# Kernel tuning notes

Hardware: AMD Instinct MI355X
Metric: run time of the kernel (lower is better)

Reference implementation:

```python
import jax, jax.numpy as jnp
from jax import lax
import numpy as np

K = 3  # kernel size for both convs


def setup_inputs() -> dict:
    key = jax.random.key(0)
    k1, k2, k3, k4, k5 = jax.random.split(key, 5)
    x = jax.random.normal(k1, (8, 3, 384, 384), dtype=jnp.float32)
    # offset-producing conv: 18 = 2*3*3 offset channels for a 3x3 deform kernel
    w1 = jax.random.normal(k2, (18, 3, K, K), dtype=jnp.float32) * 0.05
    b1 = jax.random.normal(k3, (18,), dtype=jnp.float32) * 0.05
    # deformable conv weight/bias: in=3, out=3, 3x3
    w2 = jax.random.normal(k4, (3, 3, K, K), dtype=jnp.float32) * 0.2
    b2 = jax.random.normal(k5, (3,), dtype=jnp.float32) * 0.05
    return {"x": x, "w1": w1, "b1": b1, "w2": w2, "b2": b2}


def _deform_conv2d(x, offset, w, b):
    # x: [B,C,H,W], offset: [B, 2*K*K, Ho, Wo] (per-tap (dy,dx) interleaved),
    # w: [Co,C,K,K], b: [Co]. stride=1, pad=0, dilation=1, zero-padding bilinear.
    B, C, H, W = x.shape
    KK = K * K
    Ho, Wo = H - (K - 1), W - (K - 1)
    off = offset.reshape(B, KK, 2, Ho, Wo)
    dy, dx = off[:, :, 0], off[:, :, 1]                      # [B,KK,Ho,Wo]

    kh = jnp.repeat(jnp.arange(K, dtype=jnp.float32), K)     # [KK] kernel row
    kw = jnp.tile(jnp.arange(K, dtype=jnp.float32), K)       # [KK] kernel col
    base_y = jnp.arange(Ho, dtype=jnp.float32)[None, :, None] + kh[:, None, None]  # [KK,Ho,1]
    base_x = jnp.arange(Wo, dtype=jnp.float32)[None, None, :] + kw[:, None, None]  # [KK,1,Wo]
    py = base_y[None] + dy                                   # [B,KK,Ho,Wo]
    px = base_x[None] + dx

    y0 = jnp.floor(py)
    x0 = jnp.floor(px)
    wy = py - y0
    wx = px - x0

    x_flat = x.reshape(B, C, H * W)
    N = KK * Ho * Wo

    def gather_corner(yc, xc, wgt):
        valid = (yc >= 0) & (yc <= H - 1) & (xc >= 0) & (xc <= W - 1)
        yi = jnp.clip(yc, 0, H - 1).astype(jnp.int32)
        xi = jnp.clip(xc, 0, W - 1).astype(jnp.int32)
        idx = (yi * W + xi).reshape(B, 1, N)
        g = jnp.take_along_axis(x_flat, idx, axis=2)          # [B,C,N]
        return g * (wgt * valid.astype(x.dtype)).reshape(B, 1, N)

    val = gather_corner(y0, x0, (1 - wy) * (1 - wx))
    val = val + gather_corner(y0, x0 + 1, (1 - wy) * wx)
    val = val + gather_corner(y0 + 1, x0, wy * (1 - wx))
    val = val + gather_corner(y0 + 1, x0 + 1, wy * wx)
    val = val.reshape(B, C, KK, Ho, Wo)

    out = jnp.einsum('bckhw,ock->bohw', val, w.reshape(w.shape[0], C, KK))
    return out + b[None, :, None, None]


def reference(x, w1, b1, w2, b2):
    offset = lax.conv_general_dilated(
        x, w1, window_strides=(1, 1), padding='VALID',
        dimension_numbers=('NCHW', 'OIHW', 'NCHW')) + b1[None, :, None, None]
    return _deform_conv2d(x, offset, w2, b2)
```

## Files before the change

### kernel.cpp

```cpp
#include <hip/hip_runtime.h>


#define BB 8
#define HH 384
#define WW 384
#define HO 382
#define WO 382
#define HW (HH * WW)
#define PIX_PER_BATCH (HO * WO)
#define BLOCKS_PER_BATCH ((PIX_PER_BATCH + 255) / 256)
#define TR_BLOCKS_PER_BATCH (HW / 256)

typedef float v2f __attribute__((ext_vector_type(2), aligned(4)));
typedef float v4f __attribute__((ext_vector_type(4), aligned(16)));

static __device__ __forceinline__ v2f fma2(v2f a, v2f b, v2f c) {
    return __builtin_elementwise_fma(a, b, c);
}
static __device__ __forceinline__ v4f fma4(v4f a, v4f b, v4f c) {
    return __builtin_elementwise_fma(a, b, c);
}

__global__ __launch_bounds__(256) void nchw_to_nhwc4(
    const float* __restrict__ x, v4f* __restrict__ xt)
{
    const int b    = blockIdx.x & 7;
    const int tile = blockIdx.x >> 3;
    const int idx  = tile * 256 + threadIdx.x;
    const float* xb = x + (long)b * 3 * HW;
    v4f v;
    v.x = xb[idx];
    v.y = xb[HW + idx];
    v.z = xb[2 * HW + idx];
    v.w = 0.f;
    xt[(long)b * HW + idx] = v;
}

__global__ __launch_bounds__(256, 5) void deform_fused_nhwc(
    const v4f* __restrict__ xt,
    const float* __restrict__ w1,
    const float* __restrict__ b1,
    const float* __restrict__ w2,
    const float* __restrict__ b2,
    float* __restrict__ out)
{
    __shared__ float s_w1p[486];
    __shared__ float s_b1[18];
    __shared__ float s_w2p[54];
    __shared__ float s_w2s[27];
    __shared__ float s_b2[3];

    for (int i = threadIdx.x; i < 486; i += 256) {
        const int oc = i / 27, rem = i % 27, c = rem / 9, j = rem % 9;
        const int k = oc >> 1, comp = oc & 1;
        s_w1p[((j * 3 + c) * 9 + k) * 2 + comp] = w1[i];
    }
    if (threadIdx.x < 81) {
        const int i = threadIdx.x;
        const int o = i / 27, c = (i % 27) / 9, k = i % 9;
        if (o < 2) s_w2p[(k * 3 + c) * 2 + o] = w2[i];
        else       s_w2s[k * 3 + c] = w2[i];
    }
    if (threadIdx.x < 18) s_b1[threadIdx.x] = b1[threadIdx.x];
    if (threadIdx.x < 3)  s_b2[threadIdx.x] = b2[threadIdx.x];
    __syncthreads();

    const int b    = blockIdx.x & 7;
    const int tile = blockIdx.x >> 3;
    const int idx  = tile * 256 + threadIdx.x;
    if (idx >= PIX_PER_BATCH) return;

    const int wo = idx % WO;
    const int ho = idx / WO;

    const v4f* xtb = xt + (long)b * HW;

    v2f off2[9];
#pragma unroll
    for (int k = 0; k < 9; ++k) {
        v2f v; v.x = s_b1[2 * k]; v.y = s_b1[2 * k + 1];
        off2[k] = v;
    }

    const v2f* w1p = (const v2f*)s_w1p;
#pragma unroll
    for (int j = 0; j < 9; ++j) {
        const int i = j / 3, jj = j % 3;
        const v4f q = xtb[(ho + i) * WW + (wo + jj)];
#pragma unroll
        for (int c = 0; c < 3; ++c) {
            const float xc = (c == 0) ? q.x : (c == 1) ? q.y : q.z;
            v2f xcv; xcv.x = xc; xcv.y = xc;
            const v2f* wrow = w1p + (j * 3 + c) * 9;
#pragma unroll
            for (int k = 0; k < 9; ++k)
                off2[k] = fma2(xcv, wrow[k], off2[k]);
        }
    }

    float acc0 = s_b2[0], acc1 = s_b2[1], acc2 = s_b2[2];
    const v2f* w2p = (const v2f*)s_w2p;

#pragma unroll
    for (int k = 0; k < 9; ++k) {
        const int kh = k / 3, kw = k % 3;
        v2f pos; pos.x = (float)(ho + kh); pos.y = (float)(wo + kw);
        pos += off2[k];
        const v2f fl = __builtin_elementwise_floor(pos);
        const v2f fr = pos - fl;
        const int y0 = (int)fl.x;
        const int x0 = (int)fl.y;

        const int ry0 = min(max(y0, 0), HH - 1);
        const int ry1 = min(max(y0 + 1, 0), HH - 1);
        const int xbs = min(max(x0, 0), WW - 2);

        const bool vy0 = (y0 >= 0) & (y0 <= HH - 1);
        const bool vy1 = (y0 >= -1) & (y0 <= HH - 2);
        const bool vx0 = (x0 >= 0) & (x0 <= WW - 1);
        const bool vx1 = (x0 >= -1) & (x0 <= WW - 2);
        const float wy0m = vy0 ? (1.f - fr.x) : 0.f;
        const float wy1m = vy1 ? fr.x : 0.f;
        const float wx0m = vx0 ? (1.f - fr.y) : 0.f;
        const float wx1m = vx1 ? fr.y : 0.f;

        const bool selA = (x0 >= WW - 1);
        const bool selB = (x0 >= 0);
        const float e0 = (selA ? 0.f : wx0m) + (selB ? 0.f : wx1m);
        const float e1 = (selA ? wx0m : 0.f) + (selB ? wx1m : 0.f);
        const float g00 = wy0m * e0, g01 = wy0m * e1;
        const float g10 = wy1m * e0, g11 = wy1m * e1;

        const int o0 = ry0 * WW + xbs;
        const int o1 = ry1 * WW + xbs;

        const v4f q00 = xtb[o0];
        const v4f q01 = xtb[o0 + 1];
        const v4f q10 = xtb[o1];
        const v4f q11 = xtb[o1 + 1];

        v4f gv; gv.x = g00; gv.y = g00; gv.z = g00; gv.w = g00;
        v4f t4 = gv * q00;
        gv.x = g01; gv.y = g01; gv.z = g01; gv.w = g01;
        t4 = fma4(gv, q01, t4);
        gv.x = g10; gv.y = g10; gv.z = g10; gv.w = g10;
        t4 = fma4(gv, q10, t4);
        gv.x = g11; gv.y = g11; gv.z = g11; gv.w = g11;
        t4 = fma4(gv, q11, t4);

        const float v0 = t4.x, v1 = t4.y, v2v = t4.z;

        v2f acc01; acc01.x = acc0; acc01.y = acc1;
        v2f vv;
        vv.x = v0;  vv.y = v0;  acc01 = fma2(vv, w2p[k * 3 + 0], acc01);
        vv.x = v1;  vv.y = v1;  acc01 = fma2(vv, w2p[k * 3 + 1], acc01);
        vv.x = v2v; vv.y = v2v; acc01 = fma2(vv, w2p[k * 3 + 2], acc01);
        acc0 = acc01.x; acc1 = acc01.y;
        acc2 = fmaf(s_w2s[k * 3 + 0], v0, acc2);
        acc2 = fmaf(s_w2s[k * 3 + 1], v1, acc2);
        acc2 = fmaf(s_w2s[k * 3 + 2], v2v, acc2);
    }

    const long obase = ((long)(b * 3) * HO + ho) * WO + wo;
    __builtin_nontemporal_store(acc0, out + obase);
    __builtin_nontemporal_store(acc1, out + obase + (long)HO * WO);
    __builtin_nontemporal_store(acc2, out + obase + 2L * HO * WO);
}

__global__ __launch_bounds__(256, 6) void deform_fused_fallback(
    const float* __restrict__ x,
    const float* __restrict__ w1,
    const float* __restrict__ b1,
    const float* __restrict__ w2,
    const float* __restrict__ b2,
    float* __restrict__ out)
{
    __shared__ float s_w1p[486];
    __shared__ float s_b1[18];
    __shared__ float s_w2p[54];
    __shared__ float s_w2s[27];
    __shared__ float s_b2[3];

    for (int i = threadIdx.x; i < 486; i += 256) {
        const int oc = i / 27, rem = i % 27, c = rem / 9, j = rem % 9;
        const int k = oc >> 1, comp = oc & 1;
        s_w1p[((c * 9 + j) * 9 + k) * 2 + comp] = w1[i];
    }
    if (threadIdx.x < 81) {
        const int i = threadIdx.x;
        const int o = i / 27, c = (i % 27) / 9, k = i % 9;
        if (o < 2) s_w2p[(k * 3 + c) * 2 + o] = w2[i];
        else       s_w2s[k * 3 + c] = w2[i];
    }
    if (threadIdx.x < 18) s_b1[threadIdx.x] = b1[threadIdx.x];
    if (threadIdx.x < 3)  s_b2[threadIdx.x] = b2[threadIdx.x];
    __syncthreads();

    const int b    = blockIdx.x & 7;
    const int tile = blockIdx.x >> 3;
    const int idx  = tile * 256 + threadIdx.x;
    if (idx >= PIX_PER_BATCH) return;

    const int wo = idx % WO;
    const int ho = idx / WO;

    const float* xb = x + (long)b * 3 * HW;

    v2f off2[9];
#pragma unroll
    for (int k = 0; k < 9; ++k) {
        v2f v; v.x = s_b1[2 * k]; v.y = s_b1[2 * k + 1];
        off2[k] = v;
    }

    const v2f* w1p = (const v2f*)s_w1p;
#pragma unroll
    for (int c = 0; c < 3; ++c) {
        float xr[9];
#pragma unroll
        for (int i = 0; i < 3; ++i) {
            const float* rp = xb + c * HW + (ho + i) * WW + wo;
            const v2f p = *(const v2f*)rp;
            xr[i * 3 + 0] = p.x;
            xr[i * 3 + 1] = p.y;
            xr[i * 3 + 2] = rp[2];
        }
#pragma unroll
        for (int j = 0; j < 9; ++j) {
            v2f xj; xj.x = xr[j]; xj.y = xr[j];
            const v2f* wrow = w1p + (c * 9 + j) * 9;
#pragma unroll
            for (int k = 0; k < 9; ++k)
                off2[k] = fma2(xj, wrow[k], off2[k]);
        }
    }

    float acc0 = s_b2[0], acc1 = s_b2[1], acc2 = s_b2[2];
    const float* xc0 = xb;
    const float* xc1 = xb + HW;
    const float* xc2 = xb + 2 * HW;
    const v2f* w2p = (const v2f*)s_w2p;

#pragma unroll
    for (int k = 0; k < 9; ++k) {
        const int kh = k / 3, kw = k % 3;
        v2f pos; pos.x = (float)(ho + kh); pos.y = (float)(wo + kw);
        pos += off2[k];
        const v2f fl = __builtin_elementwise_floor(pos);
        const v2f fr = pos - fl;
        const int y0 = (int)fl.x;
        const int x0 = (int)fl.y;

        const int ry0 = min(max(y0, 0), HH - 1);
        const int ry1 = min(max(y0 + 1, 0), HH - 1);
        const int xbs = min(max(x0, 0), WW - 2);

        const bool vy0 = (y0 >= 0) & (y0 <= HH - 1);
        const bool vy1 = (y0 >= -1) & (y0 <= HH - 2);
        const bool vx0 = (x0 >= 0) & (x0 <= WW - 1);
        const bool vx1 = (x0 >= -1) & (x0 <= WW - 2);
        const float wy0m = vy0 ? (1.f - fr.x) : 0.f;
        const float wy1m = vy1 ? fr.x : 0.f;
        const float wx0m = vx0 ? (1.f - fr.y) : 0.f;
        const float wx1m = vx1 ? fr.y : 0.f;

        const bool selA = (x0 >= WW - 1);
        const bool selB = (x0 >= 0);
        const float e0 = (selA ? 0.f : wx0m) + (selB ? 0.f : wx1m);
        const float e1 = (selA ? wx0m : 0.f) + (selB ? wx1m : 0.f);
        v2f f0; f0.x = wy0m * e0; f0.y = wy0m * e1;
        v2f f1; f1.x = wy1m * e0; f1.y = wy1m * e1;

        const int o0 = ry0 * WW + xbs;
        const int o1 = ry1 * WW + xbs;

        const v2f a0 = *(const v2f*)(xc0 + o0);
        const v2f a1 = *(const v2f*)(xc0 + o1);
        const v2f b0 = *(const v2f*)(xc1 + o0);
        const v2f b1v = *(const v2f*)(xc1 + o1);
        const v2f c0 = *(const v2f*)(xc2 + o0);
        const v2f c1 = *(const v2f*)(xc2 + o1);

        const v2f t0 = fma2(f1, a1, f0 * a0);
        const v2f t1 = fma2(f1, b1v, f0 * b0);
        const v2f t2 = fma2(f1, c1, f0 * c0);
        const float v0 = t0.x + t0.y;
        const float v1 = t1.x + t1.y;
        const float v2v = t2.x + t2.y;

        v2f acc01; acc01.x = acc0; acc01.y = acc1;
        v2f vv;
        vv.x = v0;  vv.y = v0;  acc01 = fma2(vv, w2p[k * 3 + 0], acc01);
        vv.x = v1;  vv.y = v1;  acc01 = fma2(vv, w2p[k * 3 + 1], acc01);
        vv.x = v2v; vv.y = v2v; acc01 = fma2(vv, w2p[k * 3 + 2], acc01);
        acc0 = acc01.x; acc1 = acc01.y;
        acc2 = fmaf(s_w2s[k * 3 + 0], v0, acc2);
        acc2 = fmaf(s_w2s[k * 3 + 1], v1, acc2);
        acc2 = fmaf(s_w2s[k * 3 + 2], v2v, acc2);
    }

    const long obase = ((long)(b * 3) * HO + ho) * WO + wo;
    __builtin_nontemporal_store(acc0, out + obase);
    __builtin_nontemporal_store(acc1, out + obase + (long)HO * WO);
    __builtin_nontemporal_store(acc2, out + obase + 2L * HO * WO);
}

extern "C" void kernel_launch(void* const* d_in, const int* in_sizes, int n_in,
                              void* d_out, int out_size, void* d_ws, size_t ws_size,
                              hipStream_t stream) {
    const float* x  = (const float*)d_in[0];
    const float* w1 = (const float*)d_in[1];
    const float* b1 = (const float*)d_in[2];
    const float* w2 = (const float*)d_in[3];
    const float* b2 = (const float*)d_in[4];
    float* out = (float*)d_out;

    const size_t need = (size_t)BB * HW * 4 * sizeof(float);
    if (ws_size >= need) {
        nchw_to_nhwc4<<<TR_BLOCKS_PER_BATCH * BB, 256, 0, stream>>>(x, (v4f*)d_ws);
        deform_fused_nhwc<<<BLOCKS_PER_BATCH * BB, 256, 0, stream>>>(
            (const v4f*)d_ws, w1, b1, w2, b2, out);
    } else {
        deform_fused_fallback<<<BLOCKS_PER_BATCH * BB, 256, 0, stream>>>(
            x, w1, b1, w2, b2, out);
    }
}
```

Baseline: 121.0 us.

## Vectorize NHWC transpose and software-pipeline bilinear tap gathers

The transpose kernel now has each thread handle four pixels, using 16-byte nontemporal loads per channel and four v4f stores, with the grid shrunk to match. The fused deform kernel prefetches the four corner gathers for the next tap while it combines the current tap, so gather latency overlaps with arithmetic. Launch bounds occupancy drops from 5 to 4 waves to leave room for the extra live registers. The trade-off is higher register pressure and lower occupancy in exchange for more memory-level parallelism per thread.

```diff
diff --git a/kernel.cpp b/kernel.cpp
--- a/kernel.cpp
+++ b/kernel.cpp
@@ -9,7 +9,7 @@
 #define HW (HH * WW)
 #define PIX_PER_BATCH (HO * WO)
 #define BLOCKS_PER_BATCH ((PIX_PER_BATCH + 255) / 256)
-#define TR_BLOCKS_PER_BATCH (HW / 256)
+#define TR_BLOCKS_PER_BATCH (HW / 1024)
 
 typedef float v2f __attribute__((ext_vector_type(2), aligned(4)));
 typedef float v4f __attribute__((ext_vector_type(4), aligned(16)));
@@ -26,17 +26,28 @@
 {
     const int b    = blockIdx.x & 7;
     const int tile = blockIdx.x >> 3;
-    const int idx  = tile * 256 + threadIdx.x;
+    const int p4   = tile * 256 + threadIdx.x;
+    const int idx  = p4 * 4;
     const float* xb = x + (long)b * 3 * HW;
-    v4f v;
-    v.x = xb[idx];
-    v.y = xb[HW + idx];
-    v.z = xb[2 * HW + idx];
-    v.w = 0.f;
-    xt[(long)b * HW + idx] = v;
-}
-
-__global__ __launch_bounds__(256, 5) void deform_fused_nhwc(
+
+    const v4f r = __builtin_nontemporal_load((const v4f*)(xb + idx));
+    const v4f g = __builtin_nontemporal_load((const v4f*)(xb + HW + idx));
+    const v4f bl = __builtin_nontemporal_load((const v4f*)(xb + 2 * HW + idx));
+
+    v4f* dst = xt + (long)b * HW + idx;
+    v4f o;
+    o.x = r.x; o.y = g.x; o.z = bl.x; o.w = 0.f; dst[0] = o;
+    o.x = r.y; o.y = g.y; o.z = bl.y;            dst[1] = o;
+    o.x = r.z; o.y = g.z; o.z = bl.z;            dst[2] = o;
+    o.x = r.w; o.y = g.w; o.z = bl.w;            dst[3] = o;
+}
+
+struct Tap {
+    v4f q00, q01, q10, q11;
+    float g00, g01, g10, g11;
+};
+
+__global__ __launch_bounds__(256, 4) void deform_fused_nhwc(
     const v4f* __restrict__ xt,
     const float* __restrict__ w1,
     const float* __restrict__ b1,
@@ -101,8 +112,7 @@
     float acc0 = s_b2[0], acc1 = s_b2[1], acc2 = s_b2[2];
     const v2f* w2p = (const v2f*)s_w2p;
 
-#pragma unroll
-    for (int k = 0; k < 9; ++k) {
+    auto prep = [&](int k) -> Tap {
         const int kh = k / 3, kw = k % 3;
         v2f pos; pos.x = (float)(ho + kh); pos.y = (float)(wo + kw);
         pos += off2[k];
@@ -128,25 +138,34 @@
         const bool selB = (x0 >= 0);
         const float e0 = (selA ? 0.f : wx0m) + (selB ? 0.f : wx1m);
         const float e1 = (selA ? wx0m : 0.f) + (selB ? wx1m : 0.f);
-        const float g00 = wy0m * e0, g01 = wy0m * e1;
-        const float g10 = wy1m * e0, g11 = wy1m * e1;
+
+        Tap t;
+        t.g00 = wy0m * e0; t.g01 = wy0m * e1;
+        t.g10 = wy1m * e0; t.g11 = wy1m * e1;
 
         const int o0 = ry0 * WW + xbs;
         const int o1 = ry1 * WW + xbs;
-
-        const v4f q00 = xtb[o0];
-        const v4f q01 = xtb[o0 + 1];
-        const v4f q10 = xtb[o1];
-        const v4f q11 = xtb[o1 + 1];
-
-        v4f gv; gv.x = g00; gv.y = g00; gv.z = g00; gv.w = g00;
-        v4f t4 = gv * q00;
-        gv.x = g01; gv.y = g01; gv.z = g01; gv.w = g01;
-        t4 = fma4(gv, q01, t4);
-        gv.x = g10; gv.y = g10; gv.z = g10; gv.w = g10;
-        t4 = fma4(gv, q10, t4);
-        gv.x = g11; gv.y = g11; gv.z = g11; gv.w = g11;
-        t4 = fma4(gv, q11, t4);
+        t.q00 = xtb[o0];
+        t.q01 = xtb[o0 + 1];
+        t.q10 = xtb[o1];
+        t.q11 = xtb[o1 + 1];
+        return t;
+    };
+
+    Tap cur = prep(0);
+#pragma unroll
+    for (int k = 0; k < 9; ++k) {
+        Tap nxt;
+        if (k < 8) nxt = prep(k + 1);
+
+        v4f gv; gv.x = cur.g00; gv.y = cur.g00; gv.z = cur.g00; gv.w = cur.g00;
+        v4f t4 = gv * cur.q00;
+        gv.x = cur.g01; gv.y = cur.g01; gv.z = cur.g01; gv.w = cur.g01;
+        t4 = fma4(gv, cur.q01, t4);
+        gv.x = cur.g10; gv.y = cur.g10; gv.z = cur.g10; gv.w = cur.g10;
+        t4 = fma4(gv, cur.q10, t4);
+        gv.x = cur.g11; gv.y = cur.g11; gv.z = cur.g11; gv.w = cur.g11;
+        t4 = fma4(gv, cur.q11, t4);
 
         const float v0 = t4.x, v1 = t4.y, v2v = t4.z;
 
@@ -159,6 +178,8 @@
         acc2 = fmaf(s_w2s[k * 3 + 0], v0, acc2);
         acc2 = fmaf(s_w2s[k * 3 + 1], v1, acc2);
         acc2 = fmaf(s_w2s[k * 3 + 2], v2v, acc2);
+
+        cur = nxt;
     }
 
     const long obase = ((long)(b * 3) * HO + ho) * WO + wo;
```

Result: slower. 126.8 us (+4.8%).
